# Optimization experiments

Measured on AMD Instinct MI355X. Metric: run time of the kernel, lower is better.

Reference implementation:

```python
import jax, jax.numpy as jnp
import numpy as np

RESO = 32          # grid_resolution
HID = 32           # hidden_dim
CDIM = 32          # c_dim
NBLK = 5           # n_blocks
PAD = 0.1          # padding
L = 10             # positional encoding frequencies -> dim 60


def setup_inputs() -> dict:
    key = jax.random.key(0)
    ks = jax.random.split(key, 12)
    B, T = 2, 200000
    p = jax.random.uniform(ks[0], (B, T, 3), jnp.float32, -0.5, 0.5)
    s = 0.05
    return {
        "p": p,
        "fc_pos_w": jax.random.normal(ks[1], (60, 2 * HID), jnp.float32) * s,
        "fc_pos_b": jax.random.normal(ks[2], (2 * HID,), jnp.float32) * s,
        "blk_fc0_w": jax.random.normal(ks[3], (NBLK, 2 * HID, HID), jnp.float32) * s,
        "blk_fc0_b": jax.random.normal(ks[4], (NBLK, HID), jnp.float32) * s,
        "blk_fc1_w": jax.random.normal(ks[5], (NBLK, HID, HID), jnp.float32) * s,
        "blk_fc1_b": jax.random.normal(ks[6], (NBLK, HID), jnp.float32) * s,
        "blk_sc_w": jax.random.normal(ks[7], (NBLK, 2 * HID, HID), jnp.float32) * s,  # shortcut, no bias
        "fc_c_w": jax.random.normal(ks[8], (HID, CDIM), jnp.float32) * s,
        "fc_c_b": jax.random.normal(ks[9], (CDIM,), jnp.float32) * s,
    }


def _pos_encode(p):
    # p in [-0.5,0.5] -> [-2,0] after 2p-1 (matches torch impl: p = 2*p - 1)
    q = 2.0 * p - 1.0
    freqs = (jnp.pi * (2.0 ** jnp.arange(L, dtype=jnp.float32)))  # [L]
    a = q[..., None, :] * freqs[:, None]                          # [B,T,L,3]
    pe = jnp.stack([jnp.sin(a), jnp.cos(a)], axis=-2)             # [B,T,L,2,3]
    return pe.reshape(*p.shape[:-1], 2 * L * 3)                   # [B,T,60]


def _normalize_3d(p):
    p_nor = p / (1.0 + PAD + 1e-3) + 0.5
    return jnp.clip(p_nor, 0.0, 1.0 - 1e-3)


def _coord2index(p_nor):
    x = jnp.floor(p_nor * RESO).astype(jnp.int32)                  # [B,T,3]
    return x[..., 0] + RESO * (x[..., 1] + RESO * x[..., 2])       # [B,T]


def _resblock(x, w0, b0, w1, b1, ws):
    h = jax.nn.relu(jax.nn.relu(x) @ w0 + b0)
    return x @ ws + (jax.nn.relu(h) @ w1 + b1)


def reference(p, fc_pos_w, fc_pos_b, blk_fc0_w, blk_fc0_b, blk_fc1_w, blk_fc1_b,
              blk_sc_w, fc_c_w, fc_c_b):
    B, T, _ = p.shape
    G = RESO ** 3
    p_nor = _normalize_3d(p)
    idx = _coord2index(p_nor)                                      # [B,T]
    gidx = (idx + jnp.arange(B, dtype=jnp.int32)[:, None] * G).reshape(-1)  # [B*T]

    net = _pos_encode(p) @ fc_pos_w + fc_pos_b                     # [B,T,64]
    net = _resblock(net, blk_fc0_w[0], blk_fc0_b[0], blk_fc1_w[0], blk_fc1_b[0], blk_sc_w[0])
    for i in range(1, NBLK):
        # pool_local: scatter_max per grid cell, gather back to points
        flat = net.reshape(B * T, HID)
        cell = jax.ops.segment_max(flat, gidx, num_segments=B * G)  # [B*G,HID]
        pooled = cell[gidx].reshape(B, T, HID)
        net = jnp.concatenate([net, pooled], axis=-1)               # [B,T,64]
        net = _resblock(net, blk_fc0_w[i], blk_fc0_b[i], blk_fc1_w[i], blk_fc1_b[i], blk_sc_w[i])

    c = net @ fc_c_w + fc_c_b                                       # [B,T,CDIM]

    # generate_grid_features: scatter_mean into grid (empty cells = 0)
    cf = c.reshape(B * T, CDIM)
    sums = jax.ops.segment_sum(cf, gidx, num_segments=B * G)        # [B*G,CDIM]
    cnt = jax.ops.segment_sum(jnp.ones((B * T, 1), c.dtype), gidx, num_segments=B * G)
    mean = sums / jnp.maximum(cnt, 1.0)
    fea_grid = mean.reshape(B, G, CDIM).transpose(0, 2, 1).reshape(B, CDIM, RESO, RESO, RESO)
    return fea_grid
```

## Files before the change

kernel.cpp:

```cpp
#include <hip/hip_runtime.h>
#include <math.h>

#define TPTS 200000
#define BB 2
#define NPTS (BB*TPTS)
#define GRID3 32768
#define BG 65536
#define SROWS 176

typedef __attribute__((ext_vector_type(8))) __bf16 bf16x8;
typedef __attribute__((ext_vector_type(4))) float f32x4;
typedef unsigned short ushort_t;

#define MFMA16(a,b,c) __builtin_amdgcn_mfma_f32_16x16x32_bf16(a,b,c,0,0,0)

__device__ __forceinline__ void split8(const float* v, bf16x8& hi, bf16x8& lo)
{
#pragma unroll
  for (int j = 0; j < 8; j++) {
    float f = v[j];
    __bf16 h = (__bf16)f;
    hi[j] = h;
    lo[j] = (__bf16)(f - (float)h);
  }
}

__device__ __forceinline__ int cellof(float p0, float p1, float p2, int t)
{
  const float DEN = (float)(1.0 + 0.1 + 1e-3);
  const float HI  = (float)(1.0 - 1e-3);
  float n0 = fminf(fmaxf(p0/DEN + 0.5f, 0.f), HI);
  float n1 = fminf(fmaxf(p1/DEN + 0.5f, 0.f), HI);
  float n2 = fminf(fmaxf(p2/DEN + 0.5f, 0.f), HI);
  int c0 = (int)floorf(n0*32.f), c1 = (int)floorf(n1*32.f), c2 = (int)floorf(n2*32.f);
  return c0 + 32*(c1 + 32*c2) + (t >= TPTS ? GRID3 : 0);
}

__global__ __launch_bounds__(256) void k_hist(
    const float* __restrict__ p, int* __restrict__ gbuf, int* __restrict__ hist)
{
  int t = blockIdx.x*256 + threadIdx.x;
  if (t >= NPTS) return;
  int g = cellof(p[3*t], p[3*t+1], p[3*t+2], t);
  gbuf[t] = g;
  atomicAdd(hist + g, 1);
}

__global__ __launch_bounds__(256) void k_scanA(
    const int* __restrict__ hist, int* __restrict__ texcl, int* __restrict__ bsum)
{
  __shared__ int sm[256];
  int tid = threadIdx.x;
  int t = blockIdx.x*256 + tid;
  int v = hist[t];
  sm[tid] = v; __syncthreads();
  for (int off = 1; off < 256; off <<= 1) {
    int x = sm[tid];
    int u = (tid >= off) ? sm[tid-off] : 0;
    __syncthreads();
    sm[tid] = x + u;
    __syncthreads();
  }
  texcl[t] = sm[tid] - v;
  if (tid == 255) bsum[blockIdx.x] = sm[255];
}

__global__ __launch_bounds__(256) void k_scanB(
    const int* __restrict__ bsum, int* __restrict__ boff)
{
  __shared__ int sm[256];
  int tid = threadIdx.x;
  int v = bsum[tid];
  sm[tid] = v; __syncthreads();
  for (int off = 1; off < 256; off <<= 1) {
    int x = sm[tid];
    int u = (tid >= off) ? sm[tid-off] : 0;
    __syncthreads();
    sm[tid] = x + u;
    __syncthreads();
  }
  boff[tid] = sm[tid] - v;
}

__global__ __launch_bounds__(256) void k_scanC(
    const int* __restrict__ texcl, const int* __restrict__ boff,
    int* __restrict__ start, int* __restrict__ cursor)
{
  int t = blockIdx.x*256 + threadIdx.x;
  int v = boff[blockIdx.x] + texcl[t];
  start[t] = v; cursor[t] = v;
  if (t == 0) start[BG] = NPTS;
}

__global__ __launch_bounds__(256) void k_scatter(
    const float* __restrict__ p, const int* __restrict__ gbuf,
    int* __restrict__ cursor, float* __restrict__ p_sorted, int* __restrict__ gsort)
{
  int t = blockIdx.x*256 + threadIdx.x;
  if (t >= NPTS) return;
  int g = gbuf[t];
  int slot = atomicAdd(cursor + g, 1);
  gsort[slot] = g;
  p_sorted[3*slot]   = p[3*t];
  p_sorted[3*slot+1] = p[3*t+1];
  p_sorted[3*slot+2] = p[3*t+2];
}

__global__ void k_pack(
    const float* __restrict__ f0w, const float* __restrict__ scw,
    const float* __restrict__ f1w, const float* __restrict__ wc,
    const float* __restrict__ Wp,
    ushort_t* __restrict__ wpack)
{
  int f = blockIdx.x, l = threadIdx.x;
  if (f >= 104) {
    int idx = f - 104;
    int c = idx >> 3, t = (idx >> 1) & 3, e = idx & 1;
#pragma unroll
    for (int j = 0; j < 8; j++) {
      int k = c*32 + (l>>4)*8 + j, n = t*16 + (l&15);
      float v = (k < 60) ? Wp[k*64 + n] : 0.f;
      __bf16 h = (__bf16)v;
      __bf16 out = (e == 0) ? h : (__bf16)(v - (float)h);
      union { __bf16 b; ushort_t u; } cv; cv.b = out;
      wpack[((size_t)f*64 + l)*8 + j] = cv.u;
    }
    return;
  }
  const float* W; int c, t, e;
  if (f < 100) {
    int s = f / 20, r = f % 20;
    if (r < 8)       { W = f0w + s*2048; c = r>>2;        t = (r>>1)&1; e = r&1; }
    else if (r < 16) { int q = r-8;  W = scw + s*2048; c = q>>2; t = (q>>1)&1; e = q&1; }
    else             { int q = r-16; W = f1w + s*1024; c = 0;    t = q>>1;     e = q&1; }
  } else { int q = f-100; W = wc; c = 0; t = q>>1; e = q&1; }
#pragma unroll
  for (int j = 0; j < 8; j++) {
    int k = c*32 + (l>>4)*8 + j, n = t*16 + (l&15);
    float v = W[k*32 + n];
    __bf16 h = (__bf16)v;
    __bf16 out = (e == 0) ? h : (__bf16)(v - (float)h);
    union { __bf16 b; ushort_t u; } cv; cv.b = out;
    wpack[((size_t)f*64 + l)*8 + j] = cv.u;
  }
}

__global__ __launch_bounds__(256) void k_fused0(
    const float* __restrict__ ps,
    const ushort_t* __restrict__ wpPE, const float* __restrict__ bp,
    const ushort_t* __restrict__ wp,
    const float* __restrict__ b0, const float* __restrict__ b1,
    float* __restrict__ net)
{
  __shared__ float xlds[4][16*68];
  __shared__ float hbuf[4][16*36];
  int wave = threadIdx.x >> 6, lane = threadIdx.x & 63;
  int m = lane & 15, q = lane >> 4;
  int pbase = (blockIdx.x*4 + wave)*16;
  int pt = pbase + m;

  float p0 = ps[3*pt], p1 = ps[3*pt+1], p2 = ps[3*pt+2];
  float u0 = 2.f*p0 - 1.f, u1 = 2.f*p1 - 1.f, u2 = 2.f*p2 - 1.f;
  const float PIF = 3.14159265358979323846f;

  float pe[2][8];
#pragma unroll
  for (int c2 = 0; c2 < 2; c2++) {
#pragma unroll
    for (int jj = 0; jj < 8; jj++) {
      int e = c2*32 + q*8 + jj;
      int l = (e * 43691) >> 18;
      int r = e - l*6;
      bool issin = (r < 3);
      int d = issin ? r : (r - 3);
      float ud = (d == 0) ? u0 : ((d == 1) ? u1 : u2);
      float xval = ldexpf(ud, l);
      float red = xval - 2.f*rintf(0.5f*xval);
      float ang = PIF*red + (issin ? 0.f : 1.5707963267948966f);
      float v = __sinf(ang);
      pe[c2][jj] = (e < 60) ? v : 0.f;
    }
  }
  bf16x8 peh[2], pel[2];
  split8(pe[0], peh[0], pel[0]);
  split8(pe[1], peh[1], pel[1]);

  f32x4 xacc[4];
#pragma unroll
  for (int t = 0; t < 4; t++) {
    float bb = bp[t*16 + m];
    xacc[t] = (f32x4){bb,bb,bb,bb};
  }
#pragma unroll
  for (int c2 = 0; c2 < 2; c2++)
#pragma unroll
    for (int t = 0; t < 4; t++) {
      bf16x8 bh = *(const bf16x8*)(wpPE + ((size_t)((c2*4+t)*2    )*64 + lane)*8);
      bf16x8 bl = *(const bf16x8*)(wpPE + ((size_t)((c2*4+t)*2 + 1)*64 + lane)*8);
      xacc[t] = MFMA16(peh[c2], bh, xacc[t]);
      xacc[t] = MFMA16(pel[c2], bh, xacc[t]);
      xacc[t] = MFMA16(peh[c2], bl, xacc[t]);
    }

  float* xl = xlds[wave];
#pragma unroll
  for (int t = 0; t < 4; t++)
#pragma unroll
    for (int r = 0; r < 4; r++)
      xl[(q*4+r)*68 + t*16 + m] = xacc[t][r];
  __syncthreads();

  float xv[2][8];
#pragma unroll
  for (int c2 = 0; c2 < 2; c2++)
#pragma unroll
    for (int jj = 0; jj < 8; jj++)
      xv[c2][jj] = xl[m*68 + c2*32 + q*8 + jj];

  bf16x8 w0f[2][2][2], wsf[2][2][2], w1f[2][2];
#pragma unroll
  for (int c = 0; c < 2; c++)
#pragma unroll
    for (int t = 0; t < 2; t++)
#pragma unroll
      for (int e = 0; e < 2; e++) {
        w0f[c][t][e] = *(const bf16x8*)(wp + ((size_t)(((c*2+t)*2+e)    )*64 + lane)*8);
        wsf[c][t][e] = *(const bf16x8*)(wp + ((size_t)(((c*2+t)*2+e) + 8)*64 + lane)*8);
      }
#pragma unroll
  for (int t = 0; t < 2; t++)
#pragma unroll
    for (int e = 0; e < 2; e++)
      w1f[t][e] = *(const bf16x8*)(wp + ((size_t)(16 + t*2 + e)*64 + lane)*8);

  bf16x8 axh[2], axl[2], arh[2], arl[2];
#pragma unroll
  for (int c = 0; c < 2; c++) {
    float r[8];
#pragma unroll
    for (int j = 0; j < 8; j++) r[j] = fmaxf(xv[c][j], 0.f);
    split8(xv[c], axh[c], axl[c]);
    split8(r,     arh[c], arl[c]);
  }

  f32x4 hacc[2], yacc[2];
#pragma unroll
  for (int t = 0; t < 2; t++) {
    float bb0 = b0[m + 16*t], bb1 = b1[m + 16*t];
    hacc[t] = (f32x4){bb0,bb0,bb0,bb0};
    yacc[t] = (f32x4){bb1,bb1,bb1,bb1};
  }

#pragma unroll
  for (int c = 0; c < 2; c++)
#pragma unroll
    for (int t = 0; t < 2; t++) {
      hacc[t] = MFMA16(arh[c], w0f[c][t][0], hacc[t]);
      hacc[t] = MFMA16(arl[c], w0f[c][t][0], hacc[t]);
      hacc[t] = MFMA16(arh[c], w0f[c][t][1], hacc[t]);
      yacc[t] = MFMA16(axh[c], wsf[c][t][0], yacc[t]);
      yacc[t] = MFMA16(axl[c], wsf[c][t][0], yacc[t]);
      yacc[t] = MFMA16(axh[c], wsf[c][t][1], yacc[t]);
    }

  float* hb = hbuf[wave];
#pragma unroll
  for (int t = 0; t < 2; t++)
#pragma unroll
    for (int r = 0; r < 4; r++)
      hb[(q*4+r)*36 + m + 16*t] = fmaxf(hacc[t][r], 0.f);
  __syncthreads();
  float hv[8];
#pragma unroll
  for (int j = 0; j < 8; j++) hv[j] = hb[m*36 + q*8 + j];
  bf16x8 hh, hl; split8(hv, hh, hl);
#pragma unroll
  for (int t = 0; t < 2; t++) {
    yacc[t] = MFMA16(hh, w1f[t][0], yacc[t]);
    yacc[t] = MFMA16(hl, w1f[t][0], yacc[t]);
    yacc[t] = MFMA16(hh, w1f[t][1], yacc[t]);
  }

#pragma unroll
  for (int t = 0; t < 2; t++)
#pragma unroll
    for (int r = 0; r < 4; r++)
      net[(size_t)(pbase + q*4 + r)*32 + m + 16*t] = yacc[t][r];
}

__global__ __launch_bounds__(256) void k_stage_f(
    const float* __restrict__ netin, float* __restrict__ netout,
    const int* __restrict__ gsort, const int* __restrict__ start,
    const ushort_t* __restrict__ wp,
    const float* __restrict__ b0, const float* __restrict__ b1)
{
  __shared__ float sbuf[SROWS*36];
  int tid = threadIdx.x;
  int P0 = blockIdx.x*64;
  int s = start[gsort[P0]];
  int e = start[gsort[P0+63] + 1];
  int n = e - s; if (n > SROWS) n = SROWS;

  for (int idx = tid; idx < n*8; idx += 256) {
    int r = idx >> 3, c = idx & 7;
    *(f32x4*)(sbuf + r*36 + c*4) =
      *(const f32x4*)(netin + ((size_t)(s + r))*32 + c*4);
  }
  __syncthreads();

  int wave = tid >> 6, lane = tid & 63;
  int m = lane & 15, q = lane >> 4;
  int pbase = P0 + wave*16;
  int pt = pbase + m;
  int g = gsort[pt];
  int cs = start[g] - s, ce = start[g+1] - s;

  float xv[2][8];
  {
    const float* xr = sbuf + (pt - s)*36 + q*8;
    *(f32x4*)&xv[0][0] = *(const f32x4*)xr;
    *(f32x4*)&xv[0][4] = *(const f32x4*)(xr + 4);
  }
  {
    f32x4 ma = (f32x4){-INFINITY,-INFINITY,-INFINITY,-INFINITY};
    f32x4 mb = ma;
    for (int k = cs; k < ce; k++) {
      const float* rr = sbuf + k*36 + q*8;
      f32x4 va = *(const f32x4*)rr;
      f32x4 vb = *(const f32x4*)(rr + 4);
      ma.x = fmaxf(ma.x, va.x); ma.y = fmaxf(ma.y, va.y);
      ma.z = fmaxf(ma.z, va.z); ma.w = fmaxf(ma.w, va.w);
      mb.x = fmaxf(mb.x, vb.x); mb.y = fmaxf(mb.y, vb.y);
      mb.z = fmaxf(mb.z, vb.z); mb.w = fmaxf(mb.w, vb.w);
    }
    *(f32x4*)&xv[1][0] = ma;
    *(f32x4*)&xv[1][4] = mb;
  }

  bf16x8 w0f[2][2][2], wsf[2][2][2], w1f[2][2];
#pragma unroll
  for (int c = 0; c < 2; c++)
#pragma unroll
    for (int t = 0; t < 2; t++)
#pragma unroll
      for (int e2 = 0; e2 < 2; e2++) {
        w0f[c][t][e2] = *(const bf16x8*)(wp + ((size_t)(((c*2+t)*2+e2)    )*64 + lane)*8);
        wsf[c][t][e2] = *(const bf16x8*)(wp + ((size_t)(((c*2+t)*2+e2) + 8)*64 + lane)*8);
      }
#pragma unroll
  for (int t = 0; t < 2; t++)
#pragma unroll
    for (int e2 = 0; e2 < 2; e2++)
      w1f[t][e2] = *(const bf16x8*)(wp + ((size_t)(16 + t*2 + e2)*64 + lane)*8);

  bf16x8 axh[2], axl[2], arh[2], arl[2];
#pragma unroll
  for (int c = 0; c < 2; c++) {
    float r[8];
#pragma unroll
    for (int j = 0; j < 8; j++) r[j] = fmaxf(xv[c][j], 0.f);
    split8(xv[c], axh[c], axl[c]);
    split8(r,     arh[c], arl[c]);
  }

  f32x4 hacc[2], yacc[2];
#pragma unroll
  for (int t = 0; t < 2; t++) {
    float bb0 = b0[m + 16*t], bb1 = b1[m + 16*t];
    hacc[t] = (f32x4){bb0,bb0,bb0,bb0};
    yacc[t] = (f32x4){bb1,bb1,bb1,bb1};
  }

#pragma unroll
  for (int c = 0; c < 2; c++)
#pragma unroll
    for (int t = 0; t < 2; t++) {
      hacc[t] = MFMA16(arh[c], w0f[c][t][0], hacc[t]);
      hacc[t] = MFMA16(arl[c], w0f[c][t][0], hacc[t]);
      hacc[t] = MFMA16(arh[c], w0f[c][t][1], hacc[t]);
      yacc[t] = MFMA16(axh[c], wsf[c][t][0], yacc[t]);
      yacc[t] = MFMA16(axl[c], wsf[c][t][0], yacc[t]);
      yacc[t] = MFMA16(axh[c], wsf[c][t][1], yacc[t]);
    }

  __syncthreads();
  float* hb = sbuf + wave*576;
#pragma unroll
  for (int t = 0; t < 2; t++)
#pragma unroll
    for (int r = 0; r < 4; r++)
      hb[(q*4+r)*36 + m + 16*t] = fmaxf(hacc[t][r], 0.f);
  __syncthreads();
  float hv[8];
#pragma unroll
  for (int j = 0; j < 8; j++) hv[j] = hb[m*36 + q*8 + j];
  bf16x8 hh, hl; split8(hv, hh, hl);
#pragma unroll
  for (int t = 0; t < 2; t++) {
    yacc[t] = MFMA16(hh, w1f[t][0], yacc[t]);
    yacc[t] = MFMA16(hl, w1f[t][0], yacc[t]);
    yacc[t] = MFMA16(hh, w1f[t][1], yacc[t]);
  }

#pragma unroll
  for (int t = 0; t < 2; t++)
#pragma unroll
    for (int r = 0; r < 4; r++)
      netout[(size_t)(pbase + q*4 + r)*32 + m + 16*t] = yacc[t][r];
}

__global__ __launch_bounds__(256) void k_final_f(
    const float* __restrict__ netin, float* __restrict__ netout,
    const int* __restrict__ gsort, const int* __restrict__ start,
    const ushort_t* __restrict__ wp, const ushort_t* __restrict__ wpc,
    const float* __restrict__ b0, const float* __restrict__ b1,
    const float* __restrict__ bc)
{
  __shared__ float sbuf[SROWS*36];
  int tid = threadIdx.x;
  int P0 = blockIdx.x*64;
  int s = start[gsort[P0]];
  int e = start[gsort[P0+63] + 1];
  int n = e - s; if (n > SROWS) n = SROWS;

  for (int idx = tid; idx < n*8; idx += 256) {
    int r = idx >> 3, c = idx & 7;
    *(f32x4*)(sbuf + r*36 + c*4) =
      *(const f32x4*)(netin + ((size_t)(s + r))*32 + c*4);
  }
  __syncthreads();

  int wave = tid >> 6, lane = tid & 63;
  int m = lane & 15, q = lane >> 4;
  int pbase = P0 + wave*16;
  int pt = pbase + m;
  int g = gsort[pt];
  int cs = start[g] - s, ce = start[g+1] - s;

  float xv[2][8];
  {
    const float* xr = sbuf + (pt - s)*36 + q*8;
    *(f32x4*)&xv[0][0] = *(const f32x4*)xr;
    *(f32x4*)&xv[0][4] = *(const f32x4*)(xr + 4);
  }
  {
    f32x4 ma = (f32x4){-INFINITY,-INFINITY,-INFINITY,-INFINITY};
    f32x4 mb = ma;
    for (int k = cs; k < ce; k++) {
      const float* rr = sbuf + k*36 + q*8;
      f32x4 va = *(const f32x4*)rr;
      f32x4 vb = *(const f32x4*)(rr + 4);
      ma.x = fmaxf(ma.x, va.x); ma.y = fmaxf(ma.y, va.y);
      ma.z = fmaxf(ma.z, va.z); ma.w = fmaxf(ma.w, va.w);
      mb.x = fmaxf(mb.x, vb.x); mb.y = fmaxf(mb.y, vb.y);
      mb.z = fmaxf(mb.z, vb.z); mb.w = fmaxf(mb.w, vb.w);
    }
    *(f32x4*)&xv[1][0] = ma;
    *(f32x4*)&xv[1][4] = mb;
  }

  bf16x8 w0f[2][2][2], wsf[2][2][2], w1f[2][2], wcf[2][2];
#pragma unroll
  for (int c = 0; c < 2; c++)
#pragma unroll
    for (int t = 0; t < 2; t++)
#pragma unroll
      for (int e2 = 0; e2 < 2; e2++) {
        w0f[c][t][e2] = *(const bf16x8*)(wp + ((size_t)(((c*2+t)*2+e2)    )*64 + lane)*8);
        wsf[c][t][e2] = *(const bf16x8*)(wp + ((size_t)(((c*2+t)*2+e2) + 8)*64 + lane)*8);
      }
#pragma unroll
  for (int t = 0; t < 2; t++)
#pragma unroll
    for (int e2 = 0; e2 < 2; e2++) {
      w1f[t][e2] = *(const bf16x8*)(wp  + ((size_t)(16 + t*2 + e2)*64 + lane)*8);
      wcf[t][e2] = *(const bf16x8*)(wpc + ((size_t)(     t*2 + e2)*64 + lane)*8);
    }

  bf16x8 axh[2], axl[2], arh[2], arl[2];
#pragma unroll
  for (int c = 0; c < 2; c++) {
    float r[8];
#pragma unroll
    for (int j = 0; j < 8; j++) r[j] = fmaxf(xv[c][j], 0.f);
    split8(xv[c], axh[c], axl[c]);
    split8(r,     arh[c], arl[c]);
  }

  f32x4 hacc[2], yacc[2];
#pragma unroll
  for (int t = 0; t < 2; t++) {
    float bb0 = b0[m + 16*t], bb1 = b1[m + 16*t];
    hacc[t] = (f32x4){bb0,bb0,bb0,bb0};
    yacc[t] = (f32x4){bb1,bb1,bb1,bb1};
  }

#pragma unroll
  for (int c = 0; c < 2; c++)
#pragma unroll
    for (int t = 0; t < 2; t++) {
      hacc[t] = MFMA16(arh[c], w0f[c][t][0], hacc[t]);
      hacc[t] = MFMA16(arl[c], w0f[c][t][0], hacc[t]);
      hacc[t] = MFMA16(arh[c], w0f[c][t][1], hacc[t]);
      yacc[t] = MFMA16(axh[c], wsf[c][t][0], yacc[t]);
      yacc[t] = MFMA16(axl[c], wsf[c][t][0], yacc[t]);
      yacc[t] = MFMA16(axh[c], wsf[c][t][1], yacc[t]);
    }

  __syncthreads();
  float* hb = sbuf + wave*576;
  float* yb = sbuf + 4*576 + wave*576;
#pragma unroll
  for (int t = 0; t < 2; t++)
#pragma unroll
    for (int r = 0; r < 4; r++)
      hb[(q*4+r)*36 + m + 16*t] = fmaxf(hacc[t][r], 0.f);
  __syncthreads();
  float hv[8];
#pragma unroll
  for (int j = 0; j < 8; j++) hv[j] = hb[m*36 + q*8 + j];
  bf16x8 hh, hl; split8(hv, hh, hl);
#pragma unroll
  for (int t = 0; t < 2; t++) {
    yacc[t] = MFMA16(hh, w1f[t][0], yacc[t]);
    yacc[t] = MFMA16(hl, w1f[t][0], yacc[t]);
    yacc[t] = MFMA16(hh, w1f[t][1], yacc[t]);
  }

#pragma unroll
  for (int t = 0; t < 2; t++)
#pragma unroll
    for (int r = 0; r < 4; r++)
      yb[(q*4+r)*36 + m + 16*t] = yacc[t][r];
  __syncthreads();
  float yv[8];
#pragma unroll
  for (int j = 0; j < 8; j++) yv[j] = yb[m*36 + q*8 + j];
  bf16x8 yh, yl; split8(yv, yh, yl);

  f32x4 cacc[2];
#pragma unroll
  for (int t = 0; t < 2; t++) {
    float bb = bc[m + 16*t];
    cacc[t] = (f32x4){bb,bb,bb,bb};
    cacc[t] = MFMA16(yh, wcf[t][0], cacc[t]);
    cacc[t] = MFMA16(yl, wcf[t][0], cacc[t]);
    cacc[t] = MFMA16(yh, wcf[t][1], cacc[t]);
  }

#pragma unroll
  for (int t = 0; t < 2; t++)
#pragma unroll
    for (int r = 0; r < 4; r++)
      netout[(size_t)(pbase + q*4 + r)*32 + m + 16*t] = cacc[t][r];
}

__global__ __launch_bounds__(256) void k_mean(
    const float* __restrict__ net, const int* __restrict__ start,
    float* __restrict__ outp)
{
  int tid = blockIdx.x*256 + threadIdx.x;
  int c = tid >> 3, sub = tid & 7;
  int s = start[c], e = start[c+1];
  f32x4 sum = (f32x4){0.f,0.f,0.f,0.f};
  for (int k = s; k < e; k++) {
    f32x4 v = *(const f32x4*)(net + (size_t)k*32 + sub*4);
    sum.x += v.x; sum.y += v.y; sum.z += v.z; sum.w += v.w;
  }
  float inv = (e > s) ? 1.f/(float)(e - s) : 0.f;
  int b = c >> 15, cell = c & 32767;
  size_t ob = ((size_t)b << 20) + cell;
#pragma unroll
  for (int jj = 0; jj < 4; jj++) {
    int ch = sub*4 + jj;
    float v = ((const float*)&sum)[jj] * inv;
    outp[ob + ((size_t)ch << 15)] = v;
  }
}

extern "C" void kernel_launch(void* const* d_in, const int* in_sizes, int n_in,
                              void* d_out, int out_size, void* d_ws, size_t ws_size,
                              hipStream_t stream)
{
  const float* p   = (const float*)d_in[0];
  const float* Wp  = (const float*)d_in[1];
  const float* bp  = (const float*)d_in[2];
  const float* f0w = (const float*)d_in[3];
  const float* f0b = (const float*)d_in[4];
  const float* f1w = (const float*)d_in[5];
  const float* f1b = (const float*)d_in[6];
  const float* scw = (const float*)d_in[7];
  const float* wc  = (const float*)d_in[8];
  const float* bc  = (const float*)d_in[9];
  float* outp = (float*)d_out;

  char* wsb = (char*)d_ws;
  float*    netA     = (float*)wsb;
  float*    netB     = netA + (size_t)NPTS*32;
  int*      gbuf     = (int*)(netB + (size_t)NPTS*32);
  int*      gsort    = gbuf + NPTS;
  int*      hist     = gsort + NPTS;
  int*      start    = hist + BG;
  int*      cursor   = start + BG + 1;
  int*      texcl    = cursor + BG;
  int*      bsum     = texcl + BG;
  int*      boff     = bsum + 256;
  ushort_t* wpack    = (ushort_t*)(boff + 256);
  float*    p_sorted = (float*)(wpack + (size_t)120*512);

  dim3 blk(256);
  dim3 gpts((NPTS + 255)/256);
  dim3 gmfma(NPTS/64);
  dim3 gcell((BG*8)/256);
  dim3 gscan(BG/256);

  hipMemsetAsync(hist, 0, (size_t)BG*4, stream);
  hipLaunchKernelGGL(k_hist, gpts, blk, 0, stream, p, gbuf, hist);
  hipLaunchKernelGGL(k_scanA, gscan, blk, 0, stream, hist, texcl, bsum);
  hipLaunchKernelGGL(k_scanB, dim3(1), blk, 0, stream, bsum, boff);
  hipLaunchKernelGGL(k_scanC, gscan, blk, 0, stream, texcl, boff, start, cursor);
  hipLaunchKernelGGL(k_scatter, gpts, blk, 0, stream, p, gbuf, cursor, p_sorted, gsort);
  hipLaunchKernelGGL(k_pack, dim3(120), dim3(64), 0, stream, f0w, scw, f1w, wc, Wp, wpack);
  hipLaunchKernelGGL(k_fused0, gmfma, blk, 0, stream,
                     p_sorted, wpack + (size_t)104*512, bp,
                     wpack + (size_t)0*20*512, f0b + 0*32, f1b + 0*32, netA);
  hipLaunchKernelGGL(k_stage_f, gmfma, blk, 0, stream, netA, netB, gsort, start,
                     wpack + (size_t)1*20*512, f0b + 1*32, f1b + 1*32);
  hipLaunchKernelGGL(k_stage_f, gmfma, blk, 0, stream, netB, netA, gsort, start,
                     wpack + (size_t)2*20*512, f0b + 2*32, f1b + 2*32);
  hipLaunchKernelGGL(k_stage_f, gmfma, blk, 0, stream, netA, netB, gsort, start,
                     wpack + (size_t)3*20*512, f0b + 3*32, f1b + 3*32);
  hipLaunchKernelGGL(k_final_f, gmfma, blk, 0, stream, netB, netA, gsort, start,
                     wpack + (size_t)4*20*512, wpack + (size_t)100*512,
                     f0b + 4*32, f1b + 4*32, bc);
  hipLaunchKernelGGL(k_mean, gcell, blk, 0, stream, netA, start, outp);
}
```

Baseline: 331.4 us.

## Fuse all per-point stages and the grid mean into one megakernel

The separate fused0, stage, final and mean kernels are replaced by a single kernel in which each 64-point block keeps the feature rows of every grid cell it touches in shared memory. Positional encoding, all five residual blocks with per-cell max pooling, fc_c and the scatter-mean run there, and the per-cell maxima are computed once per cell instead of once per point. This removes the round-trips of the 400k×32 intermediate tensors through global memory between stages, along with several launches. The cost is redundant computation of halo rows belonging to cells that span neighbouring blocks, larger shared-memory use per block, and an extra memset of the output so that empty cells read as zero.

```diff
diff --git a/kernel.cpp b/kernel.cpp
--- a/kernel.cpp
+++ b/kernel.cpp
@@ -145,93 +145,27 @@
   }
 }
 
-__global__ __launch_bounds__(256) void k_fused0(
-    const float* __restrict__ ps,
-    const ushort_t* __restrict__ wpPE, const float* __restrict__ bp,
+__device__ __forceinline__ void resblock16(
+    const float xv[2][8],
     const ushort_t* __restrict__ wp,
     const float* __restrict__ b0, const float* __restrict__ b1,
-    float* __restrict__ net)
-{
-  __shared__ float xlds[4][16*68];
-  __shared__ float hbuf[4][16*36];
-  int wave = threadIdx.x >> 6, lane = threadIdx.x & 63;
-  int m = lane & 15, q = lane >> 4;
-  int pbase = (blockIdx.x*4 + wave)*16;
-  int pt = pbase + m;
-
-  float p0 = ps[3*pt], p1 = ps[3*pt+1], p2 = ps[3*pt+2];
-  float u0 = 2.f*p0 - 1.f, u1 = 2.f*p1 - 1.f, u2 = 2.f*p2 - 1.f;
-  const float PIF = 3.14159265358979323846f;
-
-  float pe[2][8];
-#pragma unroll
-  for (int c2 = 0; c2 < 2; c2++) {
-#pragma unroll
-    for (int jj = 0; jj < 8; jj++) {
-      int e = c2*32 + q*8 + jj;
-      int l = (e * 43691) >> 18;
-      int r = e - l*6;
-      bool issin = (r < 3);
-      int d = issin ? r : (r - 3);
-      float ud = (d == 0) ? u0 : ((d == 1) ? u1 : u2);
-      float xval = ldexpf(ud, l);
-      float red = xval - 2.f*rintf(0.5f*xval);
-      float ang = PIF*red + (issin ? 0.f : 1.5707963267948966f);
-      float v = __sinf(ang);
-      pe[c2][jj] = (e < 60) ? v : 0.f;
-    }
-  }
-  bf16x8 peh[2], pel[2];
-  split8(pe[0], peh[0], pel[0]);
-  split8(pe[1], peh[1], pel[1]);
-
-  f32x4 xacc[4];
-#pragma unroll
-  for (int t = 0; t < 4; t++) {
-    float bb = bp[t*16 + m];
-    xacc[t] = (f32x4){bb,bb,bb,bb};
-  }
-#pragma unroll
-  for (int c2 = 0; c2 < 2; c2++)
-#pragma unroll
-    for (int t = 0; t < 4; t++) {
-      bf16x8 bh = *(const bf16x8*)(wpPE + ((size_t)((c2*4+t)*2    )*64 + lane)*8);
-      bf16x8 bl = *(const bf16x8*)(wpPE + ((size_t)((c2*4+t)*2 + 1)*64 + lane)*8);
-      xacc[t] = MFMA16(peh[c2], bh, xacc[t]);
-      xacc[t] = MFMA16(pel[c2], bh, xacc[t]);
-      xacc[t] = MFMA16(peh[c2], bl, xacc[t]);
-    }
-
-  float* xl = xlds[wave];
-#pragma unroll
-  for (int t = 0; t < 4; t++)
-#pragma unroll
-    for (int r = 0; r < 4; r++)
-      xl[(q*4+r)*68 + t*16 + m] = xacc[t][r];
-  __syncthreads();
-
-  float xv[2][8];
-#pragma unroll
-  for (int c2 = 0; c2 < 2; c2++)
-#pragma unroll
-    for (int jj = 0; jj < 8; jj++)
-      xv[c2][jj] = xl[m*68 + c2*32 + q*8 + jj];
-
+    int m, int q, int lane, float* hb, f32x4 yacc[2])
+{
   bf16x8 w0f[2][2][2], wsf[2][2][2], w1f[2][2];
 #pragma unroll
   for (int c = 0; c < 2; c++)
 #pragma unroll
     for (int t = 0; t < 2; t++)
 #pragma unroll
-      for (int e = 0; e < 2; e++) {
-        w0f[c][t][e] = *(const bf16x8*)(wp + ((size_t)(((c*2+t)*2+e)    )*64 + lane)*8);
-        wsf[c][t][e] = *(const bf16x8*)(wp + ((size_t)(((c*2+t)*2+e) + 8)*64 + lane)*8);
+      for (int e2 = 0; e2 < 2; e2++) {
+        w0f[c][t][e2] = *(const bf16x8*)(wp + ((size_t)(((c*2+t)*2+e2)    )*64 + lane)*8);
+        wsf[c][t][e2] = *(const bf16x8*)(wp + ((size_t)(((c*2+t)*2+e2) + 8)*64 + lane)*8);
       }
 #pragma unroll
   for (int t = 0; t < 2; t++)
 #pragma unroll
-    for (int e = 0; e < 2; e++)
-      w1f[t][e] = *(const bf16x8*)(wp + ((size_t)(16 + t*2 + e)*64 + lane)*8);
+    for (int e2 = 0; e2 < 2; e2++)
+      w1f[t][e2] = *(const bf16x8*)(wp + ((size_t)(16 + t*2 + e2)*64 + lane)*8);
 
   bf16x8 axh[2], axl[2], arh[2], arl[2];
 #pragma unroll
@@ -243,7 +177,7 @@
     split8(r,     arh[c], arl[c]);
   }
 
-  f32x4 hacc[2], yacc[2];
+  f32x4 hacc[2];
 #pragma unroll
   for (int t = 0; t < 2; t++) {
     float bb0 = b0[m + 16*t], bb1 = b1[m + 16*t];
@@ -263,13 +197,12 @@
       yacc[t] = MFMA16(axh[c], wsf[c][t][1], yacc[t]);
     }
 
-  float* hb = hbuf[wave];
 #pragma unroll
   for (int t = 0; t < 2; t++)
 #pragma unroll
-    for (int r = 0; r < 4; r++)
-      hb[(q*4+r)*36 + m + 16*t] = fmaxf(hacc[t][r], 0.f);
-  __syncthreads();
+    for (int r2 = 0; r2 < 4; r2++)
+      hb[(q*4+r2)*36 + m + 16*t] = fmaxf(hacc[t][r2], 0.f);
+  __threadfence_block();
   float hv[8];
 #pragma unroll
   for (int j = 0; j < 8; j++) hv[j] = hb[m*36 + q*8 + j];
@@ -280,301 +213,232 @@
     yacc[t] = MFMA16(hl, w1f[t][0], yacc[t]);
     yacc[t] = MFMA16(hh, w1f[t][1], yacc[t]);
   }
-
-#pragma unroll
-  for (int t = 0; t < 2; t++)
-#pragma unroll
-    for (int r = 0; r < 4; r++)
-      net[(size_t)(pbase + q*4 + r)*32 + m + 16*t] = yacc[t][r];
-}
-
-__global__ __launch_bounds__(256) void k_stage_f(
-    const float* __restrict__ netin, float* __restrict__ netout,
+}
+
+__global__ __launch_bounds__(256, 3) void k_mega(
+    const float* __restrict__ ps,
     const int* __restrict__ gsort, const int* __restrict__ start,
-    const ushort_t* __restrict__ wp,
-    const float* __restrict__ b0, const float* __restrict__ b1)
-{
-  __shared__ float sbuf[SROWS*36];
+    const ushort_t* __restrict__ wpack,
+    const float* __restrict__ bp,
+    const float* __restrict__ f0b, const float* __restrict__ f1b,
+    const float* __restrict__ bc,
+    float* __restrict__ outp)
+{
+  __shared__ float cur[SROWS*36];
+  __shared__ float scr[4608];
+  __shared__ int rowslot[SROWS];
+  __shared__ int cid[SROWS];
+  __shared__ int clist[64];
+  __shared__ int ccnt;
+
   int tid = threadIdx.x;
+  int wave = tid >> 6, lane = tid & 63;
+  int m = lane & 15, q = lane >> 4;
   int P0 = blockIdx.x*64;
   int s = start[gsort[P0]];
   int e = start[gsort[P0+63] + 1];
   int n = e - s; if (n > SROWS) n = SROWS;
-
-  for (int idx = tid; idx < n*8; idx += 256) {
-    int r = idx >> 3, c = idx & 7;
-    *(f32x4*)(sbuf + r*36 + c*4) =
-      *(const f32x4*)(netin + ((size_t)(s + r))*32 + c*4);
-  }
+  int T = (n + 15) >> 4;
+
+  if (tid == 0) ccnt = 0;
+  for (int r = tid; r < SROWS; r += 256) rowslot[r] = 0;
   __syncthreads();
-
-  int wave = tid >> 6, lane = tid & 63;
-  int m = lane & 15, q = lane >> 4;
-  int pbase = P0 + wave*16;
-  int pt = pbase + m;
-  int g = gsort[pt];
-  int cs = start[g] - s, ce = start[g+1] - s;
-
-  float xv[2][8];
+  for (int r = tid; r < n; r += 256) {
+    int cs = start[gsort[s + r]] - s;
+    rowslot[r] = cs;
+    if (cs == r) { int id = atomicAdd(&ccnt, 1); clist[id] = r; cid[r] = id; }
+  }
+  __syncthreads();
+  int nc = ccnt;
+
   {
-    const float* xr = sbuf + (pt - s)*36 + q*8;
-    *(f32x4*)&xv[0][0] = *(const f32x4*)xr;
-    *(f32x4*)&xv[0][4] = *(const f32x4*)(xr + 4);
-  }
+    const ushort_t* wpPE = wpack + (size_t)104*512;
+    const ushort_t* wp0  = wpack;
+    const float* b00 = f0b, *b10 = f1b;
+    float* xl = scr + wave*1152;
+    const float PIF = 3.14159265358979323846f;
+    for (int t = wave; t < T; t += 4) {
+      int rbase = t*16;
+      int rr = rbase + m;
+      int rsrc = (rr < n) ? rr : (n - 1);
+      const float* pp = ps + 3*(size_t)(s + rsrc);
+      float p0 = pp[0], p1 = pp[1], p2 = pp[2];
+      float u0 = 2.f*p0 - 1.f, u1 = 2.f*p1 - 1.f, u2 = 2.f*p2 - 1.f;
+
+      float pe[2][8];
+#pragma unroll
+      for (int c2 = 0; c2 < 2; c2++) {
+#pragma unroll
+        for (int jj = 0; jj < 8; jj++) {
+          int pei = c2*32 + q*8 + jj;
+          int l = (pei * 43691) >> 18;
+          int r6 = pei - l*6;
+          bool issin = (r6 < 3);
+          int d = issin ? r6 : (r6 - 3);
+          float ud = (d == 0) ? u0 : ((d == 1) ? u1 : u2);
+          float xval = ldexpf(ud, l);
+          float red = xval - 2.f*rintf(0.5f*xval);
+          float ang = PIF*red + (issin ? 0.f : 1.5707963267948966f);
+          float v = __sinf(ang);
+          pe[c2][jj] = (pei < 60) ? v : 0.f;
+        }
+      }
+      bf16x8 peh[2], pel[2];
+      split8(pe[0], peh[0], pel[0]);
+      split8(pe[1], peh[1], pel[1]);
+
+      f32x4 xacc[4];
+#pragma unroll
+      for (int tt = 0; tt < 4; tt++) {
+        float bb = bp[tt*16 + m];
+        xacc[tt] = (f32x4){bb,bb,bb,bb};
+      }
+#pragma unroll
+      for (int c2 = 0; c2 < 2; c2++)
+#pragma unroll
+        for (int tt = 0; tt < 4; tt++) {
+          bf16x8 bh = *(const bf16x8*)(wpPE + ((size_t)((c2*4+tt)*2    )*64 + lane)*8);
+          bf16x8 bl = *(const bf16x8*)(wpPE + ((size_t)((c2*4+tt)*2 + 1)*64 + lane)*8);
+          xacc[tt] = MFMA16(peh[c2], bh, xacc[tt]);
+          xacc[tt] = MFMA16(pel[c2], bh, xacc[tt]);
+          xacc[tt] = MFMA16(peh[c2], bl, xacc[tt]);
+        }
+
+#pragma unroll
+      for (int tt = 0; tt < 4; tt++)
+#pragma unroll
+        for (int r2 = 0; r2 < 4; r2++)
+          xl[(q*4+r2)*68 + tt*16 + m] = xacc[tt][r2];
+      __threadfence_block();
+      float xv[2][8];
+#pragma unroll
+      for (int c2 = 0; c2 < 2; c2++)
+#pragma unroll
+        for (int jj = 0; jj < 8; jj++)
+          xv[c2][jj] = xl[m*68 + c2*32 + q*8 + jj];
+      __threadfence_block();
+
+      f32x4 yacc[2];
+      resblock16(xv, wp0, b00, b10, m, q, lane, xl, yacc);
+
+#pragma unroll
+      for (int tt = 0; tt < 2; tt++)
+#pragma unroll
+        for (int r2 = 0; r2 < 4; r2++)
+          cur[(rbase + q*4 + r2)*36 + m + 16*tt] = yacc[tt][r2];
+    }
+  }
+  __syncthreads();
+
+  float* cmax = scr;
+  float* hbw  = scr + 2304 + wave*576;
+  for (int st = 1; st <= 4; st++) {
+    const ushort_t* wp = wpack + (size_t)st*20*512;
+    const float* b0 = f0b + st*32;
+    const float* b1 = f1b + st*32;
+
+    for (int it = tid; it < nc*4; it += 256) {
+      int ci = it >> 2, qq = it & 3;
+      int r0 = clist[ci];
+      int re = start[gsort[s + r0] + 1] - s; if (re > n) re = n;
+      f32x4 ma = (f32x4){-INFINITY,-INFINITY,-INFINITY,-INFINITY};
+      f32x4 mb = ma;
+      for (int k = r0; k < re; k++) {
+        const float* rr2 = cur + k*36 + qq*8;
+        f32x4 va = *(const f32x4*)rr2;
+        f32x4 vb = *(const f32x4*)(rr2 + 4);
+        ma.x = fmaxf(ma.x, va.x); ma.y = fmaxf(ma.y, va.y);
+        ma.z = fmaxf(ma.z, va.z); ma.w = fmaxf(ma.w, va.w);
+        mb.x = fmaxf(mb.x, vb.x); mb.y = fmaxf(mb.y, vb.y);
+        mb.z = fmaxf(mb.z, vb.z); mb.w = fmaxf(mb.w, vb.w);
+      }
+      *(f32x4*)(cmax + ci*36 + qq*8)     = ma;
+      *(f32x4*)(cmax + ci*36 + qq*8 + 4) = mb;
+    }
+    __syncthreads();
+
+    for (int t = wave; t < T; t += 4) {
+      int rbase = t*16;
+      int rr = rbase + m;
+      float xv[2][8];
+      {
+        const float* xr = cur + rr*36 + q*8;
+        *(f32x4*)&xv[0][0] = *(const f32x4*)xr;
+        *(f32x4*)&xv[0][4] = *(const f32x4*)(xr + 4);
+        int cix = cid[rowslot[rr]];
+        const float* mr = cmax + cix*36 + q*8;
+        *(f32x4*)&xv[1][0] = *(const f32x4*)mr;
+        *(f32x4*)&xv[1][4] = *(const f32x4*)(mr + 4);
+      }
+      f32x4 yacc[2];
+      resblock16(xv, wp, b0, b1, m, q, lane, hbw, yacc);
+#pragma unroll
+      for (int tt = 0; tt < 2; tt++)
+#pragma unroll
+        for (int r2 = 0; r2 < 4; r2++)
+          cur[(rbase + q*4 + r2)*36 + m + 16*tt] = yacc[tt][r2];
+    }
+    __syncthreads();
+  }
+
   {
-    f32x4 ma = (f32x4){-INFINITY,-INFINITY,-INFINITY,-INFINITY};
-    f32x4 mb = ma;
-    for (int k = cs; k < ce; k++) {
-      const float* rr = sbuf + k*36 + q*8;
-      f32x4 va = *(const f32x4*)rr;
-      f32x4 vb = *(const f32x4*)(rr + 4);
-      ma.x = fmaxf(ma.x, va.x); ma.y = fmaxf(ma.y, va.y);
-      ma.z = fmaxf(ma.z, va.z); ma.w = fmaxf(ma.w, va.w);
-      mb.x = fmaxf(mb.x, vb.x); mb.y = fmaxf(mb.y, vb.y);
-      mb.z = fmaxf(mb.z, vb.z); mb.w = fmaxf(mb.w, vb.w);
-    }
-    *(f32x4*)&xv[1][0] = ma;
-    *(f32x4*)&xv[1][4] = mb;
-  }
-
-  bf16x8 w0f[2][2][2], wsf[2][2][2], w1f[2][2];
-#pragma unroll
-  for (int c = 0; c < 2; c++)
-#pragma unroll
-    for (int t = 0; t < 2; t++)
-#pragma unroll
-      for (int e2 = 0; e2 < 2; e2++) {
-        w0f[c][t][e2] = *(const bf16x8*)(wp + ((size_t)(((c*2+t)*2+e2)    )*64 + lane)*8);
-        wsf[c][t][e2] = *(const bf16x8*)(wp + ((size_t)(((c*2+t)*2+e2) + 8)*64 + lane)*8);
-      }
-#pragma unroll
-  for (int t = 0; t < 2; t++)
-#pragma unroll
-    for (int e2 = 0; e2 < 2; e2++)
-      w1f[t][e2] = *(const bf16x8*)(wp + ((size_t)(16 + t*2 + e2)*64 + lane)*8);
-
-  bf16x8 axh[2], axl[2], arh[2], arl[2];
-#pragma unroll
-  for (int c = 0; c < 2; c++) {
-    float r[8];
-#pragma unroll
-    for (int j = 0; j < 8; j++) r[j] = fmaxf(xv[c][j], 0.f);
-    split8(xv[c], axh[c], axl[c]);
-    split8(r,     arh[c], arl[c]);
-  }
-
-  f32x4 hacc[2], yacc[2];
-#pragma unroll
-  for (int t = 0; t < 2; t++) {
-    float bb0 = b0[m + 16*t], bb1 = b1[m + 16*t];
-    hacc[t] = (f32x4){bb0,bb0,bb0,bb0};
-    yacc[t] = (f32x4){bb1,bb1,bb1,bb1};
-  }
-
-#pragma unroll
-  for (int c = 0; c < 2; c++)
-#pragma unroll
-    for (int t = 0; t < 2; t++) {
-      hacc[t] = MFMA16(arh[c], w0f[c][t][0], hacc[t]);
-      hacc[t] = MFMA16(arl[c], w0f[c][t][0], hacc[t]);
-      hacc[t] = MFMA16(arh[c], w0f[c][t][1], hacc[t]);
-      yacc[t] = MFMA16(axh[c], wsf[c][t][0], yacc[t]);
-      yacc[t] = MFMA16(axl[c], wsf[c][t][0], yacc[t]);
-      yacc[t] = MFMA16(axh[c], wsf[c][t][1], yacc[t]);
-    }
-
+    const ushort_t* wpc = wpack + (size_t)100*512;
+    bf16x8 wcf[2][2];
+#pragma unroll
+    for (int tt = 0; tt < 2; tt++)
+#pragma unroll
+      for (int e2 = 0; e2 < 2; e2++)
+        wcf[tt][e2] = *(const bf16x8*)(wpc + ((size_t)(tt*2 + e2)*64 + lane)*8);
+    for (int t = wave; t < T; t += 4) {
+      int rbase = t*16;
+      int rr = rbase + m;
+      float yv[8];
+      const float* yr = cur + rr*36 + q*8;
+      *(f32x4*)&yv[0] = *(const f32x4*)yr;
+      *(f32x4*)&yv[4] = *(const f32x4*)(yr + 4);
+      bf16x8 yh, yl; split8(yv, yh, yl);
+      f32x4 cacc[2];
+#pragma unroll
+      for (int tt = 0; tt < 2; tt++) {
+        float bb = bc[m + 16*tt];
+        cacc[tt] = (f32x4){bb,bb,bb,bb};
+        cacc[tt] = MFMA16(yh, wcf[tt][0], cacc[tt]);
+        cacc[tt] = MFMA16(yl, wcf[tt][0], cacc[tt]);
+        cacc[tt] = MFMA16(yh, wcf[tt][1], cacc[tt]);
+      }
+#pragma unroll
+      for (int tt = 0; tt < 2; tt++)
+#pragma unroll
+        for (int r2 = 0; r2 < 4; r2++)
+          cur[(rbase + q*4 + r2)*36 + m + 16*tt] = cacc[tt][r2];
+    }
+  }
   __syncthreads();
-  float* hb = sbuf + wave*576;
-#pragma unroll
-  for (int t = 0; t < 2; t++)
-#pragma unroll
-    for (int r = 0; r < 4; r++)
-      hb[(q*4+r)*36 + m + 16*t] = fmaxf(hacc[t][r], 0.f);
-  __syncthreads();
-  float hv[8];
-#pragma unroll
-  for (int j = 0; j < 8; j++) hv[j] = hb[m*36 + q*8 + j];
-  bf16x8 hh, hl; split8(hv, hh, hl);
-#pragma unroll
-  for (int t = 0; t < 2; t++) {
-    yacc[t] = MFMA16(hh, w1f[t][0], yacc[t]);
-    yacc[t] = MFMA16(hl, w1f[t][0], yacc[t]);
-    yacc[t] = MFMA16(hh, w1f[t][1], yacc[t]);
-  }
-
-#pragma unroll
-  for (int t = 0; t < 2; t++)
-#pragma unroll
-    for (int r = 0; r < 4; r++)
-      netout[(size_t)(pbase + q*4 + r)*32 + m + 16*t] = yacc[t][r];
-}
-
-__global__ __launch_bounds__(256) void k_final_f(
-    const float* __restrict__ netin, float* __restrict__ netout,
-    const int* __restrict__ gsort, const int* __restrict__ start,
-    const ushort_t* __restrict__ wp, const ushort_t* __restrict__ wpc,
-    const float* __restrict__ b0, const float* __restrict__ b1,
-    const float* __restrict__ bc)
-{
-  __shared__ float sbuf[SROWS*36];
-  int tid = threadIdx.x;
-  int P0 = blockIdx.x*64;
-  int s = start[gsort[P0]];
-  int e = start[gsort[P0+63] + 1];
-  int n = e - s; if (n > SROWS) n = SROWS;
-
-  for (int idx = tid; idx < n*8; idx += 256) {
-    int r = idx >> 3, c = idx & 7;
-    *(f32x4*)(sbuf + r*36 + c*4) =
-      *(const f32x4*)(netin + ((size_t)(s + r))*32 + c*4);
-  }
-  __syncthreads();
-
-  int wave = tid >> 6, lane = tid & 63;
-  int m = lane & 15, q = lane >> 4;
-  int pbase = P0 + wave*16;
-  int pt = pbase + m;
-  int g = gsort[pt];
-  int cs = start[g] - s, ce = start[g+1] - s;
-
-  float xv[2][8];
-  {
-    const float* xr = sbuf + (pt - s)*36 + q*8;
-    *(f32x4*)&xv[0][0] = *(const f32x4*)xr;
-    *(f32x4*)&xv[0][4] = *(const f32x4*)(xr + 4);
-  }
-  {
-    f32x4 ma = (f32x4){-INFINITY,-INFINITY,-INFINITY,-INFINITY};
-    f32x4 mb = ma;
-    for (int k = cs; k < ce; k++) {
-      const float* rr = sbuf + k*36 + q*8;
-      f32x4 va = *(const f32x4*)rr;
-      f32x4 vb = *(const f32x4*)(rr + 4);
-      ma.x = fmaxf(ma.x, va.x); ma.y = fmaxf(ma.y, va.y);
-      ma.z = fmaxf(ma.z, va.z); ma.w = fmaxf(ma.w, va.w);
-      mb.x = fmaxf(mb.x, vb.x); mb.y = fmaxf(mb.y, vb.y);
-      mb.z = fmaxf(mb.z, vb.z); mb.w = fmaxf(mb.w, vb.w);
-    }
-    *(f32x4*)&xv[1][0] = ma;
-    *(f32x4*)&xv[1][4] = mb;
-  }
-
-  bf16x8 w0f[2][2][2], wsf[2][2][2], w1f[2][2], wcf[2][2];
-#pragma unroll
-  for (int c = 0; c < 2; c++)
-#pragma unroll
-    for (int t = 0; t < 2; t++)
-#pragma unroll
-      for (int e2 = 0; e2 < 2; e2++) {
-        w0f[c][t][e2] = *(const bf16x8*)(wp + ((size_t)(((c*2+t)*2+e2)    )*64 + lane)*8);
-        wsf[c][t][e2] = *(const bf16x8*)(wp + ((size_t)(((c*2+t)*2+e2) + 8)*64 + lane)*8);
-      }
-#pragma unroll
-  for (int t = 0; t < 2; t++)
-#pragma unroll
-    for (int e2 = 0; e2 < 2; e2++) {
-      w1f[t][e2] = *(const bf16x8*)(wp  + ((size_t)(16 + t*2 + e2)*64 + lane)*8);
-      wcf[t][e2] = *(const bf16x8*)(wpc + ((size_t)(     t*2 + e2)*64 + lane)*8);
-    }
-
-  bf16x8 axh[2], axl[2], arh[2], arl[2];
-#pragma unroll
-  for (int c = 0; c < 2; c++) {
-    float r[8];
-#pragma unroll
-    for (int j = 0; j < 8; j++) r[j] = fmaxf(xv[c][j], 0.f);
-    split8(xv[c], axh[c], axl[c]);
-    split8(r,     arh[c], arl[c]);
-  }
-
-  f32x4 hacc[2], yacc[2];
-#pragma unroll
-  for (int t = 0; t < 2; t++) {
-    float bb0 = b0[m + 16*t], bb1 = b1[m + 16*t];
-    hacc[t] = (f32x4){bb0,bb0,bb0,bb0};
-    yacc[t] = (f32x4){bb1,bb1,bb1,bb1};
-  }
-
-#pragma unroll
-  for (int c = 0; c < 2; c++)
-#pragma unroll
-    for (int t = 0; t < 2; t++) {
-      hacc[t] = MFMA16(arh[c], w0f[c][t][0], hacc[t]);
-      hacc[t] = MFMA16(arl[c], w0f[c][t][0], hacc[t]);
-      hacc[t] = MFMA16(arh[c], w0f[c][t][1], hacc[t]);
-      yacc[t] = MFMA16(axh[c], wsf[c][t][0], yacc[t]);
-      yacc[t] = MFMA16(axl[c], wsf[c][t][0], yacc[t]);
-      yacc[t] = MFMA16(axh[c], wsf[c][t][1], yacc[t]);
-    }
-
-  __syncthreads();
-  float* hb = sbuf + wave*576;
-  float* yb = sbuf + 4*576 + wave*576;
-#pragma unroll
-  for (int t = 0; t < 2; t++)
-#pragma unroll
-    for (int r = 0; r < 4; r++)
-      hb[(q*4+r)*36 + m + 16*t] = fmaxf(hacc[t][r], 0.f);
-  __syncthreads();
-  float hv[8];
-#pragma unroll
-  for (int j = 0; j < 8; j++) hv[j] = hb[m*36 + q*8 + j];
-  bf16x8 hh, hl; split8(hv, hh, hl);
-#pragma unroll
-  for (int t = 0; t < 2; t++) {
-    yacc[t] = MFMA16(hh, w1f[t][0], yacc[t]);
-    yacc[t] = MFMA16(hl, w1f[t][0], yacc[t]);
-    yacc[t] = MFMA16(hh, w1f[t][1], yacc[t]);
-  }
-
-#pragma unroll
-  for (int t = 0; t < 2; t++)
-#pragma unroll
-    for (int r = 0; r < 4; r++)
-      yb[(q*4+r)*36 + m + 16*t] = yacc[t][r];
-  __syncthreads();
-  float yv[8];
-#pragma unroll
-  for (int j = 0; j < 8; j++) yv[j] = yb[m*36 + q*8 + j];
-  bf16x8 yh, yl; split8(yv, yh, yl);
-
-  f32x4 cacc[2];
-#pragma unroll
-  for (int t = 0; t < 2; t++) {
-    float bb = bc[m + 16*t];
-    cacc[t] = (f32x4){bb,bb,bb,bb};
-    cacc[t] = MFMA16(yh, wcf[t][0], cacc[t]);
-    cacc[t] = MFMA16(yl, wcf[t][0], cacc[t]);
-    cacc[t] = MFMA16(yh, wcf[t][1], cacc[t]);
-  }
-
-#pragma unroll
-  for (int t = 0; t < 2; t++)
-#pragma unroll
-    for (int r = 0; r < 4; r++)
-      netout[(size_t)(pbase + q*4 + r)*32 + m + 16*t] = cacc[t][r];
-}
-
-__global__ __launch_bounds__(256) void k_mean(
-    const float* __restrict__ net, const int* __restrict__ start,
-    float* __restrict__ outp)
-{
-  int tid = blockIdx.x*256 + threadIdx.x;
-  int c = tid >> 3, sub = tid & 7;
-  int s = start[c], e = start[c+1];
-  f32x4 sum = (f32x4){0.f,0.f,0.f,0.f};
-  for (int k = s; k < e; k++) {
-    f32x4 v = *(const f32x4*)(net + (size_t)k*32 + sub*4);
-    sum.x += v.x; sum.y += v.y; sum.z += v.z; sum.w += v.w;
-  }
-  float inv = (e > s) ? 1.f/(float)(e - s) : 0.f;
-  int b = c >> 15, cell = c & 32767;
-  size_t ob = ((size_t)b << 20) + cell;
-#pragma unroll
-  for (int jj = 0; jj < 4; jj++) {
-    int ch = sub*4 + jj;
-    float v = ((const float*)&sum)[jj] * inv;
-    outp[ob + ((size_t)ch << 15)] = v;
+
+  int rlo = P0 - s;
+  for (int it = tid; it < nc*4; it += 256) {
+    int ci = it >> 2, qq = it & 3;
+    int r0 = clist[ci];
+    if (r0 < rlo || r0 >= rlo + 64) continue;
+    int g = gsort[s + r0];
+    int re = start[g + 1] - s; if (re > n) re = n;
+    f32x4 sa = (f32x4){0.f,0.f,0.f,0.f};
+    f32x4 sb = sa;
+    for (int k = r0; k < re; k++) {
+      const float* rr2 = cur + k*36 + qq*8;
+      f32x4 va = *(const f32x4*)rr2;
+      f32x4 vb = *(const f32x4*)(rr2 + 4);
+      sa.x += va.x; sa.y += va.y; sa.z += va.z; sa.w += va.w;
+      sb.x += vb.x; sb.y += vb.y; sb.z += vb.z; sb.w += vb.w;
+    }
+    float inv = 1.f / (float)(re - r0);
+    int b = g >> 15, cell = g & 32767;
+    size_t ob = ((size_t)b << 20) + cell;
+#pragma unroll
+    for (int jj = 0; jj < 4; jj++) {
+      outp[ob + ((size_t)(qq*8 + jj)     << 15)] = ((const float*)&sa)[jj] * inv;
+      outp[ob + ((size_t)(qq*8 + jj + 4) << 15)] = ((const float*)&sb)[jj] * inv;
+    }
   }
 }
 
@@ -595,9 +459,7 @@
   float* outp = (float*)d_out;
 
   char* wsb = (char*)d_ws;
-  float*    netA     = (float*)wsb;
-  float*    netB     = netA + (size_t)NPTS*32;
-  int*      gbuf     = (int*)(netB + (size_t)NPTS*32);
+  int*      gbuf     = (int*)wsb;
   int*      gsort    = gbuf + NPTS;
   int*      hist     = gsort + NPTS;
   int*      start    = hist + BG;
@@ -610,28 +472,17 @@
 
   dim3 blk(256);
   dim3 gpts((NPTS + 255)/256);
-  dim3 gmfma(NPTS/64);
-  dim3 gcell((BG*8)/256);
+  dim3 gmega(NPTS/64);
   dim3 gscan(BG/256);
 
   hipMemsetAsync(hist, 0, (size_t)BG*4, stream);
+  hipMemsetAsync(outp, 0, (size_t)BG*32*4, stream);
   hipLaunchKernelGGL(k_hist, gpts, blk, 0, stream, p, gbuf, hist);
   hipLaunchKernelGGL(k_scanA, gscan, blk, 0, stream, hist, texcl, bsum);
   hipLaunchKernelGGL(k_scanB, dim3(1), blk, 0, stream, bsum, boff);
   hipLaunchKernelGGL(k_scanC, gscan, blk, 0, stream, texcl, boff, start, cursor);
   hipLaunchKernelGGL(k_scatter, gpts, blk, 0, stream, p, gbuf, cursor, p_sorted, gsort);
   hipLaunchKernelGGL(k_pack, dim3(120), dim3(64), 0, stream, f0w, scw, f1w, wc, Wp, wpack);
-  hipLaunchKernelGGL(k_fused0, gmfma, blk, 0, stream,
-                     p_sorted, wpack + (size_t)104*512, bp,
-                     wpack + (size_t)0*20*512, f0b + 0*32, f1b + 0*32, netA);
-  hipLaunchKernelGGL(k_stage_f, gmfma, blk, 0, stream, netA, netB, gsort, start,
-                     wpack + (size_t)1*20*512, f0b + 1*32, f1b + 1*32);
-  hipLaunchKernelGGL(k_stage_f, gmfma, blk, 0, stream, netB, netA, gsort, start,
-                     wpack + (size_t)2*20*512, f0b + 2*32, f1b + 2*32);
-  hipLaunchKernelGGL(k_stage_f, gmfma, blk, 0, stream, netA, netB, gsort, start,
-                     wpack + (size_t)3*20*512, f0b + 3*32, f1b + 3*32);
-  hipLaunchKernelGGL(k_final_f, gmfma, blk, 0, stream, netB, netA, gsort, start,
-                     wpack + (size_t)4*20*512, wpack + (size_t)100*512,
-                     f0b + 4*32, f1b + 4*32, bc);
-  hipLaunchKernelGGL(k_mean, gcell, blk, 0, stream, netA, start, outp);
-}
+  hipLaunchKernelGGL(k_mega, gmega, blk, 0, stream,
+                     p_sorted, gsort, start, wpack, bp, f0b, f1b, bc, outp);
+}
```

Measured after the change: 583.0 us. +75.9%, slower.
